# Kernel optimization log

Measured on AMD Instinct MI355X. Metric: run time of the kernel, lower is better.

Reference implementation:

```python
import jax, jax.numpy as jnp
import numpy as np

K = 1.0            # curvature (manifold.k); sqrt(K)=1 simplifies formulas
EPS = 1e-5         # module eps used in variance rescale
MIN_NORM = 1e-8    # clamp for sqrt of Lorentz inners
MAX_EUCLID = 10.0  # rescale_to_max_euclid cap (keeps cosh/sinh in fp32 range)


def l_inner(x, y):
    # Lorentz inner product <x,y>_L = -x0*y0 + <x_s, y_s>, keepdim
    return -x[..., :1] * y[..., :1] + jnp.sum(x[..., 1:] * y[..., 1:], axis=-1, keepdims=True)


def centroid(x):
    # Lorentzian centroid over the group axis (dim=-2)
    avg = jnp.mean(x, axis=-2, keepdims=True)
    denom = jnp.sqrt(jnp.clip(-l_inner(avg, avg), MIN_NORM, None))
    return avg / denom


def logmap(x, y):
    alpha = jnp.clip(-l_inner(x, y), 1.0 + 1e-7, None)   # -<x,y>_L >= 1
    dist = jnp.arccosh(alpha)
    nomin = y - alpha * x                                # y + <x,y>_L * x
    denom = jnp.sqrt(jnp.clip(l_inner(nomin, nomin), MIN_NORM, None))
    return dist * nomin / denom


def _plus_origin(p):
    # p + o where o = (1, 0, ..., 0)
    return jnp.concatenate([p[..., :1] + 1.0, p[..., 1:]], axis=-1)


def transp0back(x, v):
    # parallel transport of tangent v at x back to the origin o
    nom = -v[..., :1]                 # <o, v>_L = -v0
    denom = 1.0 + x[..., :1]          # K - <x, o>_L = 1 + x0
    return v + (nom / denom) * _plus_origin(x)


def transp0(y, v):
    # parallel transport of tangent v at origin o to point y
    nom = l_inner(y, v)
    denom = 1.0 + y[..., :1]          # K - <o, y>_L = 1 + y0
    return v + (nom / denom) * _plus_origin(y)


def rescale_to_max_euclid(u):
    n = jnp.linalg.norm(u, axis=-1, keepdims=True)
    scale = jnp.minimum(1.0, MAX_EUCLID / jnp.clip(n, MIN_NORM, None))
    return u * scale


def expmap(x, u):
    nrm = jnp.sqrt(jnp.clip(l_inner(u, u), MIN_NORM, None))
    return jnp.cosh(nrm) * x + jnp.sinh(nrm) * (u / nrm)


def setup_inputs() -> dict:
    key = jax.random.key(0)
    k1, = jax.random.split(key, 1)
    bs, h, w, c = 64, 56, 56, 128
    # sample spatial components, lift onto the hyperboloid: x0 = sqrt(1+|xs|^2)
    xs = 0.5 * jax.random.normal(k1, (bs, h, w, c - 1), dtype=jnp.float32)
    x0 = jnp.sqrt(1.0 + jnp.sum(xs * xs, axis=-1, keepdims=True))
    x = jnp.concatenate([x0, xs], axis=-1)
    gamma = jnp.ones((c,), dtype=jnp.float32)
    # beta = manifold.origin(c) = (1, 0, ..., 0)
    beta = jnp.zeros((c,), dtype=jnp.float32).at[0].set(1.0)
    return {"x": x, "gamma": gamma, "beta": beta, "groups": 8}


def reference(x, gamma, beta, groups):
    bs, h, w, c = x.shape
    xg = x.reshape(bs, -1, groups, c)                    # (bs, hw/g, g, c)
    mean = centroid(xg)                                  # (bs, hw/g, 1, c)
    x_T = logmap(mean, xg)                               # tangent at mean
    x_T = transp0back(mean, x_T)                         # tangent at origin
    # Frechet-style variance: mean Euclidean norm over spatial dim (dim=1)
    var = jnp.mean(jnp.linalg.norm(x_T, axis=-1, keepdims=True), axis=1, keepdims=True)
    x_T = x_T * (gamma / (var + EPS))
    x_T = rescale_to_max_euclid(x_T)
    x_T = transp0(beta, x_T)                             # transport to beta
    out = expmap(beta, x_T)
    return out.reshape(bs, h, w, c)
```

## Files before the change

kernel.cpp:

```cpp
#include <hip/hip_runtime.h>
#include <math.h>


constexpr int S_GROUPS = 392;
constexpr int N_GROUPS = 64 * S_GROUPS;
constexpr int CSTRIDE = 192;

__device__ __forceinline__ void wave_lds_fence() {
  __asm__ volatile("" ::: "memory");
  __builtin_amdgcn_wave_barrier();
  __asm__ volatile("" ::: "memory");
}

__device__ __forceinline__ void rsum8x3(float& a, float& b, float& c) {
#pragma unroll
  for (int m = 1; m <= 4; m <<= 1) {
    a += __shfl_xor(a, m, 64);
    b += __shfl_xor(b, m, 64);
    c += __shfl_xor(c, m, 64);
  }
}

__device__ __forceinline__ void fold_mean(const float v[16], int lane,
                                          float& c0, float& c1) {
  float a8[8];
  const bool h5 = (lane & 32) != 0;
#pragma unroll
  for (int i = 0; i < 8; ++i) {
    float kp = h5 ? v[i + 8] : v[i];
    float sd = h5 ? v[i] : v[i + 8];
    a8[i] = kp + __shfl_xor(sd, 32, 64);
  }
  float a4[4];
  const bool h4 = (lane & 16) != 0;
#pragma unroll
  for (int i = 0; i < 4; ++i) {
    float kp = h4 ? a8[i + 4] : a8[i];
    float sd = h4 ? a8[i] : a8[i + 4];
    a4[i] = kp + __shfl_xor(sd, 16, 64);
  }
  const bool h3 = (lane & 8) != 0;
  float kp0 = h3 ? a4[2] : a4[0], sd0 = h3 ? a4[0] : a4[2];
  float kp1 = h3 ? a4[3] : a4[1], sd1 = h3 ? a4[1] : a4[3];
  c0 = (kp0 + __shfl_xor(sd0, 8, 64)) * 0.125f;
  c1 = (kp1 + __shfl_xor(sd1, 8, 64)) * 0.125f;
}

struct CoreOut {
  float avg[16];
  float sc, k, coef;
  float nvar;
};

__device__ __forceinline__ void core(const float v[16], const float gm[16],
                                     const float bt[16], int lane,
                                     float* __restrict__ smrow,
                                     float* __restrict__ gc, CoreOut& o) {
  const int p = lane >> 3, q = lane & 7;
  float c0, c1;
  fold_mean(v, lane, c0, c1);
  *reinterpret_cast<float2*>(&smrow[q * 16 + p * 2]) = make_float2(c0, c1);
  *reinterpret_cast<float2*>(&gc[q * 16 + p * 2]) = make_float2(c0, c1);
  wave_lds_fence();
#pragma unroll
  for (int j = 0; j < 4; ++j)
    *reinterpret_cast<float4*>(&o.avg[4 * j]) =
        *reinterpret_cast<const float4*>(&smrow[q * 16 + 4 * j]);
  wave_lds_fence();

  float pa = 0.f, pd = 0.f, py = 0.f;
#pragma unroll
  for (int i = 0; i < 16; ++i) {
    pa = fmaf(o.avg[i], o.avg[i], pa);
    pd = fmaf(o.avg[i], v[i], pd);
    py = fmaf(v[i], v[i], py);
  }
  if (q == 0) {
    pa -= 2.f * o.avg[0] * o.avg[0];
    pd -= 2.f * o.avg[0] * v[0];
  }
  rsum8x3(pa, pd, py);
  const float y0p = __shfl(v[0], lane & 56, 64);
  const float avg0 = __shfl(o.avg[0], 0, 64);

  float rden = rsqrtf(fmaxf(-pa, 1e-8f));
  float a_raw = -pd * rden;
  float alpha = fmaxf(a_raw, 1.f + 1e-7f);
  float t = alpha - 1.f;
  float dist = log1pf(t + sqrtf(t * (alpha + 1.f)));
  float yyL = py - 2.f * y0p * y0p;
  float inn = fmaxf(yyL + 2.f * alpha * a_raw - alpha * alpha, 1e-8f);
  o.sc = dist * rsqrtf(inn);
  float am = alpha * rden;
  float mean0 = rden * avg0;
  float v0 = o.sc * (y0p - am * avg0);
  o.coef = -v0 / (1.f + mean0);
  o.k = o.coef * rden - o.sc * am;

  float na = 0.f, pe = 0.f, pb = 0.f, xt0 = 0.f, gx0 = 0.f;
#pragma unroll
  for (int i = 0; i < 16; ++i) {
    float xt = fmaf(o.sc, v[i], o.k * o.avg[i]);
    if (i == 0) xt += (q == 0) ? o.coef : 0.f;
    float gx = gm[i] * xt;
    na = fmaf(xt, xt, na);
    pe = fmaf(gx, gx, pe);
    pb = fmaf(bt[i], gx, pb);
    if (i == 0) { xt0 = xt; gx0 = gx; }
  }
  if (q == 0) pb -= 2.f * bt[0] * gx0;
  rsum8x3(na, pe, pb);
  o.nvar = sqrtf(na);
  if (q == 0) {
    *reinterpret_cast<float4*>(&gc[128 + p * 8]) =
        make_float4(o.sc, o.k, o.coef, pe);
    *reinterpret_cast<float4*>(&gc[128 + p * 8 + 4]) =
        make_float4(pb, xt0, 0.f, 0.f);
  }
}

__global__ __launch_bounds__(256) void lngn_pass1(
    const float* __restrict__ x, const float* __restrict__ gamma,
    const float* __restrict__ beta, float* __restrict__ var_part,
    float* __restrict__ cache) {
  __shared__ float sm[4][2][128];
  const int w = threadIdx.x >> 6, lane = threadIdx.x & 63;
  const int p = lane >> 3, q = lane & 7;
  const int wid0 = (blockIdx.x * 4 + w) * 2;
  const float* b0 = x + (size_t)wid0 * 1024 + p * 128 + q * 16;
  float vA[16], vB[16], gm[16], bt[16];
#pragma unroll
  for (int j = 0; j < 4; ++j) {
    *reinterpret_cast<float4*>(&vA[4 * j]) =
        *reinterpret_cast<const float4*>(b0 + 4 * j);
    *reinterpret_cast<float4*>(&vB[4 * j]) =
        *reinterpret_cast<const float4*>(b0 + 1024 + 4 * j);
    *reinterpret_cast<float4*>(&gm[4 * j]) =
        *reinterpret_cast<const float4*>(gamma + q * 16 + 4 * j);
    *reinterpret_cast<float4*>(&bt[4 * j]) =
        *reinterpret_cast<const float4*>(beta + q * 16 + 4 * j);
  }
  CoreOut A, B;
  core(vA, gm, bt, lane, sm[w][0], cache + (size_t)wid0 * CSTRIDE, A);
  core(vB, gm, bt, lane, sm[w][1], cache + (size_t)(wid0 + 1) * CSTRIDE, B);
  if (q == 0) {
    const int b = wid0 / S_GROUPS;
    const int s = wid0 - b * S_GROUPS;
    var_part[(size_t)(b * 8 + p) * S_GROUPS + s] = A.nvar;
    var_part[(size_t)(b * 8 + p) * S_GROUPS + s + 1] = B.nvar;
  }
}

__global__ __launch_bounds__(256) void lngn_finalize(
    const float* __restrict__ var_part, const float* __restrict__ beta,
    float* __restrict__ var_out) {
  const int wv = (int)((blockIdx.x * 256 + threadIdx.x) >> 6);
  const int lane = threadIdx.x & 63;
  const float* base = var_part + (size_t)wv * S_GROUPS;
  float s = 0.f;
  for (int s0 = lane; s0 < S_GROUPS; s0 += 64) s += base[s0];
#pragma unroll
  for (int m = 32; m >= 1; m >>= 1) s += __shfl_xor(s, m, 64);
  if (lane == 0) var_out[wv] = s * (1.f / (float)S_GROUPS);

  if (blockIdx.x == 0 && threadIdx.x < 64) {
    const int l = threadIdx.x;
    float b0v = beta[2 * l], b1v = beta[2 * l + 1];
    float tsum = b0v * b0v + b1v * b1v;
    if (l == 0) tsum -= 2.f * b0v * b0v;
#pragma unroll
    for (int m = 32; m >= 1; m >>= 1) tsum += __shfl_xor(tsum, m, 64);
    if (l == 0) var_out[512] = tsum;
  }
}

__global__ __launch_bounds__(256) void lngn_pass2(
    const float* __restrict__ x, const float* __restrict__ gamma,
    const float* __restrict__ beta, const float* __restrict__ var,
    const float* __restrict__ cache, float* __restrict__ out) {
  const int w = threadIdx.x >> 6, lane = threadIdx.x & 63;
  const int wid = blockIdx.x * 4 + w;
  const float* xb = x + (size_t)wid * 1024;
  const float* gc = cache + (size_t)wid * CSTRIDE;
  const int cl = lane & 31;
  const int par = lane >> 5;

  float4 xv[4];
#pragma unroll
  for (int j = 0; j < 4; ++j)
    xv[j] = *reinterpret_cast<const float4*>(xb + j * 256 + 4 * lane);
  const float4 av = *reinterpret_cast<const float4*>(gc + 4 * cl);
  const float4 gm4 = *reinterpret_cast<const float4*>(gamma + 4 * cl);
  const float4 bt4 = *reinterpret_cast<const float4*>(beta + 4 * cl);

  const int pix = lane & 7;
  const float4 s0 = *reinterpret_cast<const float4*>(gc + 128 + pix * 8);
  const float4 s1v = *reinterpret_cast<const float4*>(gc + 128 + pix * 8 + 4);
  const float sc = s0.x, kk = s0.y, coef = s0.z, PE = s0.w;
  const float PB = s1v.x, XT0 = s1v.y;
  const int b = wid / S_GROUPS;
  const float varv = var[b * 8 + pix];
  const float pbb = var[512];
  const float bt0 = beta[0], gm0 = gamma[0];

  const float is1 = 1.f / (varv + 1e-5f);
  const float pe = is1 * is1 * PE;
  const float pb = is1 * PB;
  const float u0 = is1 * gm0 * XT0;
  const float n = sqrtf(pe);
  const float scl = fminf(1.f, 10.f / fmaxf(n, 1e-8f));
  const float c2 = scl * pb / (1.f + bt0);
  const float uuL = pe - 2.f * u0 * u0;
  const float innw = scl * scl * uuL + 2.f * scl * c2 * (pb - u0) +
                     c2 * c2 * (pbb - 2.f * bt0 - 1.f);
  const float nrm = sqrtf(fmaxf(innw, 1e-8f));
  const float e = expf(nrm), ie = 1.f / e;
  const float chv = 0.5f * (e + ie);
  const float isn = (0.5f * (e - ie)) / nrm;
  const float A1 = chv + isn * c2;
  const float Cu = isn * scl * is1;
  const float A2 = Cu * sc;
  const float A3 = Cu * kk;
  const float A4 = fmaf(Cu * gm0, coef, isn * c2);

  float* ob = out + (size_t)wid * 1024;
#pragma unroll
  for (int j = 0; j < 4; ++j) {
    const int sp = 2 * j + par;
    const float a1 = __shfl(A1, sp, 64);
    const float a2 = __shfl(A2, sp, 64);
    const float a3 = __shfl(A3, sp, 64);
    const float a4 = __shfl(A4, sp, 64);
    float4 o4;
    o4.x = fmaf(a1, bt4.x, gm4.x * fmaf(a2, xv[j].x, a3 * av.x));
    o4.y = fmaf(a1, bt4.y, gm4.y * fmaf(a2, xv[j].y, a3 * av.y));
    o4.z = fmaf(a1, bt4.z, gm4.z * fmaf(a2, xv[j].z, a3 * av.z));
    o4.w = fmaf(a1, bt4.w, gm4.w * fmaf(a2, xv[j].w, a3 * av.w));
    if (cl == 0) o4.x += a4;
    *reinterpret_cast<float4*>(ob + j * 256 + 4 * lane) = o4;
  }
}

extern "C" void kernel_launch(void* const* d_in, const int* in_sizes, int n_in,
                              void* d_out, int out_size, void* d_ws,
                              size_t ws_size, hipStream_t stream) {
  const float* x = (const float*)d_in[0];
  const float* gamma = (const float*)d_in[1];
  const float* beta = (const float*)d_in[2];
  float* out = (float*)d_out;
  float* var_part = (float*)d_ws;
  float* var_final = var_part + (size_t)N_GROUPS * 8;
  float* cache = var_part + 201472;

  lngn_pass1<<<N_GROUPS / 8, 256, 0, stream>>>(x, gamma, beta, var_part, cache);
  lngn_finalize<<<128, 256, 0, stream>>>(var_part, beta, var_final);
  lngn_pass2<<<N_GROUPS / 4, 256, 0, stream>>>(x, gamma, beta, var_final, cache,
                                               out);
}
```

Before: 208.6 us.

## Remap pass1 lanes to channel-parallel layout, drop LDS transpose and shuffles

Changes pass1's thread mapping so each lane holds four channels of four pixels (channel-parallel), making the group mean a single cross-half shuffle instead of a multi-stage fold plus an LDS round trip. The per-pixel tangent norm is computed algebraically from the dot products rather than from a second pass over elements. It removes LDS traffic and wave barriers but adds more shuffle reductions (5 steps over many values) and raises register pressure. The loads become fully coalesced float4 accesses.

New measurement: 219.3 us. 1.05x slower.

```diff
diff --git a/kernel.cpp b/kernel.cpp
--- a/kernel.cpp
+++ b/kernel.cpp
@@ -6,10 +6,8 @@
 constexpr int N_GROUPS = 64 * S_GROUPS;
 constexpr int CSTRIDE = 192;
 
-__device__ __forceinline__ void wave_lds_fence() {
-  __asm__ volatile("" ::: "memory");
-  __builtin_amdgcn_wave_barrier();
-  __asm__ volatile("" ::: "memory");
+__device__ __forceinline__ float dot4(const float4 a, const float4 b) {
+  return fmaf(a.x, b.x, fmaf(a.y, b.y, fmaf(a.z, b.z, a.w * b.w)));
 }
 
 __device__ __forceinline__ void rsum8x3(float& a, float& b, float& c) {
@@ -21,101 +19,104 @@
   }
 }
 
-__device__ __forceinline__ void fold_mean(const float v[16], int lane,
-                                          float& c0, float& c1) {
-  float a8[8];
-  const bool h5 = (lane & 32) != 0;
-#pragma unroll
-  for (int i = 0; i < 8; ++i) {
-    float kp = h5 ? v[i + 8] : v[i];
-    float sd = h5 ? v[i] : v[i + 8];
-    a8[i] = kp + __shfl_xor(sd, 32, 64);
-  }
-  float a4[4];
-  const bool h4 = (lane & 16) != 0;
-#pragma unroll
-  for (int i = 0; i < 4; ++i) {
-    float kp = h4 ? a8[i + 4] : a8[i];
-    float sd = h4 ? a8[i] : a8[i + 4];
-    a4[i] = kp + __shfl_xor(sd, 16, 64);
-  }
-  const bool h3 = (lane & 8) != 0;
-  float kp0 = h3 ? a4[2] : a4[0], sd0 = h3 ? a4[0] : a4[2];
-  float kp1 = h3 ? a4[3] : a4[1], sd1 = h3 ? a4[1] : a4[3];
-  c0 = (kp0 + __shfl_xor(sd0, 8, 64)) * 0.125f;
-  c1 = (kp1 + __shfl_xor(sd1, 8, 64)) * 0.125f;
-}
-
-struct CoreOut {
-  float avg[16];
-  float sc, k, coef;
-  float nvar;
-};
-
-__device__ __forceinline__ void core(const float v[16], const float gm[16],
-                                     const float bt[16], int lane,
-                                     float* __restrict__ smrow,
-                                     float* __restrict__ gc, CoreOut& o) {
-  const int p = lane >> 3, q = lane & 7;
-  float c0, c1;
-  fold_mean(v, lane, c0, c1);
-  *reinterpret_cast<float2*>(&smrow[q * 16 + p * 2]) = make_float2(c0, c1);
-  *reinterpret_cast<float2*>(&gc[q * 16 + p * 2]) = make_float2(c0, c1);
-  wave_lds_fence();
+__device__ __forceinline__ void core_cp(
+    const float4 v[4], const float4 gm4, const float4 bt4, const float4 g24,
+    const float4 bg4, float gm0, float bt0, int c, int par,
+    float* __restrict__ gc, float* __restrict__ var_part, int b, int s) {
+  float4 sum;
+  sum.x = v[0].x + v[1].x + v[2].x + v[3].x;
+  sum.y = v[0].y + v[1].y + v[2].y + v[3].y;
+  sum.z = v[0].z + v[1].z + v[2].z + v[3].z;
+  sum.w = v[0].w + v[1].w + v[2].w + v[3].w;
+  float4 avg;
+  avg.x = (sum.x + __shfl_xor(sum.x, 32, 64)) * 0.125f;
+  avg.y = (sum.y + __shfl_xor(sum.y, 32, 64)) * 0.125f;
+  avg.z = (sum.z + __shfl_xor(sum.z, 32, 64)) * 0.125f;
+  avg.w = (sum.w + __shfl_xor(sum.w, 32, 64)) * 0.125f;
+  if (par == 0)
+    *reinterpret_cast<float4*>(gc + 4 * c) = avg;
+
+  float aa = dot4(avg, avg);
+  float ya[4], yy[4];
+#pragma unroll
+  for (int j = 0; j < 4; ++j) {
+    ya[j] = dot4(avg, v[j]);
+    yy[j] = dot4(v[j], v[j]);
+  }
+#pragma unroll
+  for (int m = 1; m <= 16; m <<= 1) {
+    aa += __shfl_xor(aa, m, 64);
+#pragma unroll
+    for (int j = 0; j < 4; ++j) {
+      ya[j] += __shfl_xor(ya[j], m, 64);
+      yy[j] += __shfl_xor(yy[j], m, 64);
+    }
+  }
+  const float avg0 = __shfl(avg.x, 0, 64);
+  float y0[4];
 #pragma unroll
   for (int j = 0; j < 4; ++j)
-    *reinterpret_cast<float4*>(&o.avg[4 * j]) =
-        *reinterpret_cast<const float4*>(&smrow[q * 16 + 4 * j]);
-  wave_lds_fence();
-
-  float pa = 0.f, pd = 0.f, py = 0.f;
-#pragma unroll
-  for (int i = 0; i < 16; ++i) {
-    pa = fmaf(o.avg[i], o.avg[i], pa);
-    pd = fmaf(o.avg[i], v[i], pd);
-    py = fmaf(v[i], v[i], py);
-  }
-  if (q == 0) {
-    pa -= 2.f * o.avg[0] * o.avg[0];
-    pd -= 2.f * o.avg[0] * v[0];
-  }
-  rsum8x3(pa, pd, py);
-  const float y0p = __shfl(v[0], lane & 56, 64);
-  const float avg0 = __shfl(o.avg[0], 0, 64);
-
-  float rden = rsqrtf(fmaxf(-pa, 1e-8f));
-  float a_raw = -pd * rden;
-  float alpha = fmaxf(a_raw, 1.f + 1e-7f);
-  float t = alpha - 1.f;
-  float dist = log1pf(t + sqrtf(t * (alpha + 1.f)));
-  float yyL = py - 2.f * y0p * y0p;
-  float inn = fmaxf(yyL + 2.f * alpha * a_raw - alpha * alpha, 1e-8f);
-  o.sc = dist * rsqrtf(inn);
-  float am = alpha * rden;
-  float mean0 = rden * avg0;
-  float v0 = o.sc * (y0p - am * avg0);
-  o.coef = -v0 / (1.f + mean0);
-  o.k = o.coef * rden - o.sc * am;
-
-  float na = 0.f, pe = 0.f, pb = 0.f, xt0 = 0.f, gx0 = 0.f;
-#pragma unroll
-  for (int i = 0; i < 16; ++i) {
-    float xt = fmaf(o.sc, v[i], o.k * o.avg[i]);
-    if (i == 0) xt += (q == 0) ? o.coef : 0.f;
-    float gx = gm[i] * xt;
-    na = fmaf(xt, xt, na);
-    pe = fmaf(gx, gx, pe);
-    pb = fmaf(bt[i], gx, pb);
-    if (i == 0) { xt0 = xt; gx0 = gx; }
-  }
-  if (q == 0) pb -= 2.f * bt[0] * gx0;
-  rsum8x3(na, pe, pb);
-  o.nvar = sqrtf(na);
-  if (q == 0) {
-    *reinterpret_cast<float4*>(&gc[128 + p * 8]) =
-        make_float4(o.sc, o.k, o.coef, pe);
-    *reinterpret_cast<float4*>(&gc[128 + p * 8 + 4]) =
-        make_float4(pb, xt0, 0.f, 0.f);
+    y0[j] = __shfl(v[j].x, par * 32, 64);
+
+  const float aaL = aa - 2.f * avg0 * avg0;
+  const float rden = rsqrtf(fmaxf(-aaL, 1e-8f));
+  const float mean0 = rden * avg0;
+  float scv[4], kv[4], cfv[4], xt0v[4];
+#pragma unroll
+  for (int j = 0; j < 4; ++j) {
+    const float yaL = ya[j] - 2.f * avg0 * y0[j];
+    const float yyL = yy[j] - 2.f * y0[j] * y0[j];
+    const float a_raw = -yaL * rden;
+    const float alpha = fmaxf(a_raw, 1.f + 1e-7f);
+    const float t = alpha - 1.f;
+    const float dist = log1pf(t + sqrtf(t * (alpha + 1.f)));
+    const float inn = fmaxf(yyL + 2.f * alpha * a_raw - alpha * alpha, 1e-8f);
+    const float sc = dist * rsqrtf(inn);
+    const float am = alpha * rden;
+    const float v0 = sc * (y0[j] - am * avg0);
+    const float coef = -v0 / (1.f + mean0);
+    const float k = coef * rden - sc * am;
+    scv[j] = sc; kv[j] = k; cfv[j] = coef;
+    const float T0 = fmaf(sc, y0[j], k * avg0);
+    const float na = sc * sc * yy[j] + k * k * aa + 2.f * sc * k * ya[j] +
+                     coef * coef + 2.f * coef * T0;
+    xt0v[j] = T0 + coef;
+    const float nvar = sqrtf(fmaxf(na, 0.f));
+    if (c == j)
+      var_part[(size_t)(b * 8 + 2 * j + par) * S_GROUPS + s] = nvar;
+  }
+
+  float pe[4], pb[4];
+#pragma unroll
+  for (int j = 0; j < 4; ++j) {
+    float4 xt;
+    xt.x = fmaf(scv[j], v[j].x, kv[j] * avg.x);
+    xt.y = fmaf(scv[j], v[j].y, kv[j] * avg.y);
+    xt.z = fmaf(scv[j], v[j].z, kv[j] * avg.z);
+    xt.w = fmaf(scv[j], v[j].w, kv[j] * avg.w);
+    if (c == 0) xt.x += cfv[j];
+    pe[j] = g24.x * xt.x * xt.x + g24.y * xt.y * xt.y + g24.z * xt.z * xt.z +
+            g24.w * xt.w * xt.w;
+    pb[j] = dot4(bg4, xt);
+  }
+#pragma unroll
+  for (int m = 1; m <= 16; m <<= 1) {
+#pragma unroll
+    for (int j = 0; j < 4; ++j) {
+      pe[j] += __shfl_xor(pe[j], m, 64);
+      pb[j] += __shfl_xor(pb[j], m, 64);
+    }
+  }
+#pragma unroll
+  for (int j = 0; j < 4; ++j) {
+    const float PB = pb[j] - 2.f * bt0 * (gm0 * xt0v[j]);
+    if (c == j) {
+      const int pix = 2 * j + par;
+      *reinterpret_cast<float4*>(gc + 128 + pix * 8) =
+          make_float4(scv[j], kv[j], cfv[j], pe[j]);
+      *reinterpret_cast<float4*>(gc + 128 + pix * 8 + 4) =
+          make_float4(PB, xt0v[j], 0.f, 0.f);
+    }
   }
 }
 
@@ -123,32 +124,32 @@
     const float* __restrict__ x, const float* __restrict__ gamma,
     const float* __restrict__ beta, float* __restrict__ var_part,
     float* __restrict__ cache) {
-  __shared__ float sm[4][2][128];
   const int w = threadIdx.x >> 6, lane = threadIdx.x & 63;
-  const int p = lane >> 3, q = lane & 7;
+  const int c = lane & 31, par = lane >> 5;
   const int wid0 = (blockIdx.x * 4 + w) * 2;
-  const float* b0 = x + (size_t)wid0 * 1024 + p * 128 + q * 16;
-  float vA[16], vB[16], gm[16], bt[16];
-#pragma unroll
-  for (int j = 0; j < 4; ++j) {
-    *reinterpret_cast<float4*>(&vA[4 * j]) =
-        *reinterpret_cast<const float4*>(b0 + 4 * j);
-    *reinterpret_cast<float4*>(&vB[4 * j]) =
-        *reinterpret_cast<const float4*>(b0 + 1024 + 4 * j);
-    *reinterpret_cast<float4*>(&gm[4 * j]) =
-        *reinterpret_cast<const float4*>(gamma + q * 16 + 4 * j);
-    *reinterpret_cast<float4*>(&bt[4 * j]) =
-        *reinterpret_cast<const float4*>(beta + q * 16 + 4 * j);
-  }
-  CoreOut A, B;
-  core(vA, gm, bt, lane, sm[w][0], cache + (size_t)wid0 * CSTRIDE, A);
-  core(vB, gm, bt, lane, sm[w][1], cache + (size_t)(wid0 + 1) * CSTRIDE, B);
-  if (q == 0) {
-    const int b = wid0 / S_GROUPS;
-    const int s = wid0 - b * S_GROUPS;
-    var_part[(size_t)(b * 8 + p) * S_GROUPS + s] = A.nvar;
-    var_part[(size_t)(b * 8 + p) * S_GROUPS + s + 1] = B.nvar;
-  }
+  const float* g0 = x + (size_t)wid0 * 1024;
+
+  float4 vA[4], vB[4];
+#pragma unroll
+  for (int j = 0; j < 4; ++j) {
+    vA[j] = *reinterpret_cast<const float4*>(g0 + j * 256 + 4 * lane);
+    vB[j] = *reinterpret_cast<const float4*>(g0 + 1024 + j * 256 + 4 * lane);
+  }
+  const float4 gm4 = *reinterpret_cast<const float4*>(gamma + 4 * c);
+  const float4 bt4 = *reinterpret_cast<const float4*>(beta + 4 * c);
+  float4 g24, bg4;
+  g24.x = gm4.x * gm4.x; g24.y = gm4.y * gm4.y;
+  g24.z = gm4.z * gm4.z; g24.w = gm4.w * gm4.w;
+  bg4.x = bt4.x * gm4.x; bg4.y = bt4.y * gm4.y;
+  bg4.z = bt4.z * gm4.z; bg4.w = bt4.w * gm4.w;
+  const float gm0 = gamma[0], bt0 = beta[0];
+
+  const int b = wid0 / S_GROUPS;
+  const int s = wid0 - b * S_GROUPS;
+  core_cp(vA, gm4, bt4, g24, bg4, gm0, bt0, c, par,
+          cache + (size_t)wid0 * CSTRIDE, var_part, b, s);
+  core_cp(vB, gm4, bt4, g24, bg4, gm0, bt0, c, par,
+          cache + (size_t)(wid0 + 1) * CSTRIDE, var_part, b, s + 1);
 }
 
 __global__ __launch_bounds__(256) void lngn_finalize(
```

## Precompute all dot products in one pass and derive norms algebraically

Applied to the files above, without the earlier changes.

Pass 1 now gathers eight dot products per group (plain, gamma-weighted and beta-weighted) in a single loop over the loaded values. It then derives the tangent-vector norm, weighted norm and beta projection in closed form from those scalars, instead of building x_T and doing a second reduction. The two groups per wave are interleaved to expose more independent work. This removes the second shuffle-reduction chain and a serialized dependency, at the cost of more registers and possible cancellation error in the expanded quadratic forms.

New measurement: 209.7 us. About the same (+0.5%).

```diff
diff --git a/kernel.cpp b/kernel.cpp
--- a/kernel.cpp
+++ b/kernel.cpp
@@ -10,15 +10,6 @@
   __asm__ volatile("" ::: "memory");
   __builtin_amdgcn_wave_barrier();
   __asm__ volatile("" ::: "memory");
-}
-
-__device__ __forceinline__ void rsum8x3(float& a, float& b, float& c) {
-#pragma unroll
-  for (int m = 1; m <= 4; m <<= 1) {
-    a += __shfl_xor(a, m, 64);
-    b += __shfl_xor(b, m, 64);
-    c += __shfl_xor(c, m, 64);
-  }
 }
 
 __device__ __forceinline__ void fold_mean(const float v[16], int lane,
@@ -46,76 +37,43 @@
   c1 = (kp1 + __shfl_xor(sd1, 8, 64)) * 0.125f;
 }
 
-struct CoreOut {
-  float avg[16];
-  float sc, k, coef;
-  float nvar;
+struct Dots {
+  float pa, pd, py, Gyy, Gya, Gaa, By, Ba;
 };
 
-__device__ __forceinline__ void core(const float v[16], const float gm[16],
-                                     const float bt[16], int lane,
-                                     float* __restrict__ smrow,
-                                     float* __restrict__ gc, CoreOut& o) {
-  const int p = lane >> 3, q = lane & 7;
-  float c0, c1;
-  fold_mean(v, lane, c0, c1);
-  *reinterpret_cast<float2*>(&smrow[q * 16 + p * 2]) = make_float2(c0, c1);
-  *reinterpret_cast<float2*>(&gc[q * 16 + p * 2]) = make_float2(c0, c1);
-  wave_lds_fence();
-#pragma unroll
-  for (int j = 0; j < 4; ++j)
-    *reinterpret_cast<float4*>(&o.avg[4 * j]) =
-        *reinterpret_cast<const float4*>(&smrow[q * 16 + 4 * j]);
-  wave_lds_fence();
-
-  float pa = 0.f, pd = 0.f, py = 0.f;
-#pragma unroll
-  for (int i = 0; i < 16; ++i) {
-    pa = fmaf(o.avg[i], o.avg[i], pa);
-    pd = fmaf(o.avg[i], v[i], pd);
-    py = fmaf(v[i], v[i], py);
-  }
+__device__ __forceinline__ void chain_ep(const Dots& d, float y0, float avg0,
+                                         float gm0, float b0g0, int q, int p,
+                                         float* __restrict__ gc,
+                                         float* __restrict__ var_part,
+                                         size_t vidx) {
+  const float aaL = d.pa - 2.f * avg0 * avg0;
+  const float rden = rsqrtf(fmaxf(-aaL, 1e-8f));
+  const float mean0 = rden * avg0;
+  const float yaL = d.pd - 2.f * avg0 * y0;
+  const float yyL = d.py - 2.f * y0 * y0;
+  const float a_raw = -yaL * rden;
+  const float alpha = fmaxf(a_raw, 1.f + 1e-7f);
+  const float t = alpha - 1.f;
+  const float dist = log1pf(t + sqrtf(t * (alpha + 1.f)));
+  const float inn = fmaxf(yyL + 2.f * alpha * a_raw - alpha * alpha, 1e-8f);
+  const float sc = dist * rsqrtf(inn);
+  const float am = alpha * rden;
+  const float v0 = sc * (y0 - am * avg0);
+  const float coef = -v0 / (1.f + mean0);
+  const float k = coef * rden - sc * am;
+  const float T0 = fmaf(sc, y0, k * avg0);
+  const float na = sc * sc * d.py + k * k * d.pa + 2.f * sc * k * d.pd +
+                   coef * coef + 2.f * coef * T0;
+  const float nvar = sqrtf(fmaxf(na, 0.f));
+  const float pe = sc * sc * d.Gyy + k * k * d.Gaa + 2.f * sc * k * d.Gya +
+                   gm0 * gm0 * coef * (coef + 2.f * T0);
+  const float pb = fmaf(sc, d.By, k * d.Ba) - b0g0 * (2.f * T0 + coef);
+  const float XT0 = T0 + coef;
   if (q == 0) {
-    pa -= 2.f * o.avg[0] * o.avg[0];
-    pd -= 2.f * o.avg[0] * v[0];
-  }
-  rsum8x3(pa, pd, py);
-  const float y0p = __shfl(v[0], lane & 56, 64);
-  const float avg0 = __shfl(o.avg[0], 0, 64);
-
-  float rden = rsqrtf(fmaxf(-pa, 1e-8f));
-  float a_raw = -pd * rden;
-  float alpha = fmaxf(a_raw, 1.f + 1e-7f);
-  float t = alpha - 1.f;
-  float dist = log1pf(t + sqrtf(t * (alpha + 1.f)));
-  float yyL = py - 2.f * y0p * y0p;
-  float inn = fmaxf(yyL + 2.f * alpha * a_raw - alpha * alpha, 1e-8f);
-  o.sc = dist * rsqrtf(inn);
-  float am = alpha * rden;
-  float mean0 = rden * avg0;
-  float v0 = o.sc * (y0p - am * avg0);
-  o.coef = -v0 / (1.f + mean0);
-  o.k = o.coef * rden - o.sc * am;
-
-  float na = 0.f, pe = 0.f, pb = 0.f, xt0 = 0.f, gx0 = 0.f;
-#pragma unroll
-  for (int i = 0; i < 16; ++i) {
-    float xt = fmaf(o.sc, v[i], o.k * o.avg[i]);
-    if (i == 0) xt += (q == 0) ? o.coef : 0.f;
-    float gx = gm[i] * xt;
-    na = fmaf(xt, xt, na);
-    pe = fmaf(gx, gx, pe);
-    pb = fmaf(bt[i], gx, pb);
-    if (i == 0) { xt0 = xt; gx0 = gx; }
-  }
-  if (q == 0) pb -= 2.f * bt[0] * gx0;
-  rsum8x3(na, pe, pb);
-  o.nvar = sqrtf(na);
-  if (q == 0) {
-    *reinterpret_cast<float4*>(&gc[128 + p * 8]) =
-        make_float4(o.sc, o.k, o.coef, pe);
-    *reinterpret_cast<float4*>(&gc[128 + p * 8 + 4]) =
-        make_float4(pb, xt0, 0.f, 0.f);
+    *reinterpret_cast<float4*>(gc + 128 + p * 8) = make_float4(sc, k, coef, pe);
+    *reinterpret_cast<float4*>(gc + 128 + p * 8 + 4) =
+        make_float4(pb, XT0, 0.f, 0.f);
+    var_part[vidx] = nvar;
   }
 }
 
@@ -128,6 +86,9 @@
   const int p = lane >> 3, q = lane & 7;
   const int wid0 = (blockIdx.x * 4 + w) * 2;
   const float* b0 = x + (size_t)wid0 * 1024 + p * 128 + q * 16;
+  float* gcA = cache + (size_t)wid0 * CSTRIDE;
+  float* gcB = gcA + CSTRIDE;
+
   float vA[16], vB[16], gm[16], bt[16];
 #pragma unroll
   for (int j = 0; j < 4; ++j) {
@@ -140,15 +101,70 @@
     *reinterpret_cast<float4*>(&bt[4 * j]) =
         *reinterpret_cast<const float4*>(beta + q * 16 + 4 * j);
   }
-  CoreOut A, B;
-  core(vA, gm, bt, lane, sm[w][0], cache + (size_t)wid0 * CSTRIDE, A);
-  core(vB, gm, bt, lane, sm[w][1], cache + (size_t)(wid0 + 1) * CSTRIDE, B);
-  if (q == 0) {
-    const int b = wid0 / S_GROUPS;
-    const int s = wid0 - b * S_GROUPS;
-    var_part[(size_t)(b * 8 + p) * S_GROUPS + s] = A.nvar;
-    var_part[(size_t)(b * 8 + p) * S_GROUPS + s + 1] = B.nvar;
-  }
+
+  float c0A, c1A, c0B, c1B;
+  fold_mean(vA, lane, c0A, c1A);
+  fold_mean(vB, lane, c0B, c1B);
+  *reinterpret_cast<float2*>(&sm[w][0][q * 16 + p * 2]) = make_float2(c0A, c1A);
+  *reinterpret_cast<float2*>(&sm[w][1][q * 16 + p * 2]) = make_float2(c0B, c1B);
+  *reinterpret_cast<float2*>(&gcA[q * 16 + p * 2]) = make_float2(c0A, c1A);
+  *reinterpret_cast<float2*>(&gcB[q * 16 + p * 2]) = make_float2(c0B, c1B);
+  wave_lds_fence();
+  float avgA[16], avgB[16];
+#pragma unroll
+  for (int j = 0; j < 4; ++j) {
+    *reinterpret_cast<float4*>(&avgA[4 * j]) =
+        *reinterpret_cast<const float4*>(&sm[w][0][q * 16 + 4 * j]);
+    *reinterpret_cast<float4*>(&avgB[4 * j]) =
+        *reinterpret_cast<const float4*>(&sm[w][1][q * 16 + 4 * j]);
+  }
+  wave_lds_fence();
+
+  Dots A = {0, 0, 0, 0, 0, 0, 0, 0}, B = {0, 0, 0, 0, 0, 0, 0, 0};
+#pragma unroll
+  for (int i = 0; i < 16; ++i) {
+    const float gyA = gm[i] * vA[i], gaA = gm[i] * avgA[i];
+    A.pa = fmaf(avgA[i], avgA[i], A.pa);
+    A.pd = fmaf(avgA[i], vA[i], A.pd);
+    A.py = fmaf(vA[i], vA[i], A.py);
+    A.Gyy = fmaf(gyA, gyA, A.Gyy);
+    A.Gya = fmaf(gyA, gaA, A.Gya);
+    A.Gaa = fmaf(gaA, gaA, A.Gaa);
+    A.By = fmaf(bt[i], gyA, A.By);
+    A.Ba = fmaf(bt[i], gaA, A.Ba);
+    const float gyB = gm[i] * vB[i], gaB = gm[i] * avgB[i];
+    B.pa = fmaf(avgB[i], avgB[i], B.pa);
+    B.pd = fmaf(avgB[i], vB[i], B.pd);
+    B.py = fmaf(vB[i], vB[i], B.py);
+    B.Gyy = fmaf(gyB, gyB, B.Gyy);
+    B.Gya = fmaf(gyB, gaB, B.Gya);
+    B.Gaa = fmaf(gaB, gaB, B.Gaa);
+    B.By = fmaf(bt[i], gyB, B.By);
+    B.Ba = fmaf(bt[i], gaB, B.Ba);
+  }
+#pragma unroll
+  for (int m = 1; m <= 4; m <<= 1) {
+    A.pa += __shfl_xor(A.pa, m, 64);   B.pa += __shfl_xor(B.pa, m, 64);
+    A.pd += __shfl_xor(A.pd, m, 64);   B.pd += __shfl_xor(B.pd, m, 64);
+    A.py += __shfl_xor(A.py, m, 64);   B.py += __shfl_xor(B.py, m, 64);
+    A.Gyy += __shfl_xor(A.Gyy, m, 64); B.Gyy += __shfl_xor(B.Gyy, m, 64);
+    A.Gya += __shfl_xor(A.Gya, m, 64); B.Gya += __shfl_xor(B.Gya, m, 64);
+    A.Gaa += __shfl_xor(A.Gaa, m, 64); B.Gaa += __shfl_xor(B.Gaa, m, 64);
+    A.By += __shfl_xor(A.By, m, 64);   B.By += __shfl_xor(B.By, m, 64);
+    A.Ba += __shfl_xor(A.Ba, m, 64);   B.Ba += __shfl_xor(B.Ba, m, 64);
+  }
+  const float y0A = __shfl(vA[0], lane & 56, 64);
+  const float y0B = __shfl(vB[0], lane & 56, 64);
+  const float avg0A = __shfl(avgA[0], 0, 64);
+  const float avg0B = __shfl(avgB[0], 0, 64);
+  const float gm0 = gamma[0], b0g0 = beta[0] * gamma[0];
+
+  const int b = wid0 / S_GROUPS;
+  const int s = wid0 - b * S_GROUPS;
+  chain_ep(A, y0A, avg0A, gm0, b0g0, q, p, gcA, var_part,
+           (size_t)(b * 8 + p) * S_GROUPS + s);
+  chain_ep(B, y0B, avg0B, gm0, b0g0, q, p, gcB, var_part,
+           (size_t)(b * 8 + p) * S_GROUPS + s + 1);
 }
 
 __global__ __launch_bounds__(256) void lngn_finalize(
```
